# Performance work log

Hardware: AMD Instinct MI355X
Metric: run time of the kernel (lower is better)

The kernel has to match this reference:

```python
import jax, jax.numpy as jnp
import numpy as np

B, Q, S1, S2 = 4, 256, 2048, 2048   # batch, latents, kv lengths
D, H, K, F = 2048, 16, 128, 8192    # embed_dim, heads, key_size, ffn dim
LN_EPS = 1e-5


def _layer_norm(x, scale, offset):
    mu = jnp.mean(x, axis=-1, keepdims=True)
    var = jnp.var(x, axis=-1, keepdims=True)
    return (x - mu) * jax.lax.rsqrt(var + LN_EPS) * scale + offset


def _cross_attention(q_in, kv_in, wq, bq, wk, bk, wv, bv, wo, bo, bias_k, bias_v):
    b, q_len, _ = q_in.shape
    t = kv_in.shape[1]
    qh = (q_in @ wq + bq).reshape(b, q_len, H, K)
    kh = (kv_in @ wk + bk).reshape(b, t, H, K)
    vh = (kv_in @ wv + bv).reshape(b, t, H, K)
    # ESM-style learned bias key/value appended as one extra kv position
    kh = jnp.concatenate([kh, jnp.broadcast_to(bias_k, (b, 1, H, K))], axis=1)
    vh = jnp.concatenate([vh, jnp.broadcast_to(bias_v, (b, 1, H, K))], axis=1)
    scale = jnp.sqrt(jnp.asarray(K, q_in.dtype))
    logits = jnp.einsum('bqhk,bthk->bhqt', qh, kh) / scale  # [B,H,Q,T+1]
    weights = jax.nn.softmax(logits, axis=-1)
    ctx = jnp.einsum('bhqt,bthk->bqhk', weights, vh).reshape(b, q_len, H * K)
    return ctx @ wo + bo


def _forward(x, xf_1, xf_2,
             ln1_scale, ln1_offset, wq1, bq1, wk1, bk1, wv1, bv1, wo1, bo1, bias_k1, bias_v1,
             ln2_scale, ln2_offset, wq2, bq2, wk2, bk2, wv2, bv2, wo2, bo2, bias_k2, bias_v2,
             ln_mlp_scale, ln_mlp_offset, w_fc1, b_fc1, w_fc2, b_fc2):
    res = x
    h = _layer_norm(x, ln1_scale, ln1_offset)
    x = res + _cross_attention(h, xf_1, wq1, bq1, wk1, bk1, wv1, bv1, wo1, bo1, bias_k1, bias_v1)
    res = x
    h = _layer_norm(x, ln2_scale, ln2_offset)
    x = res + _cross_attention(h, xf_2, wq2, bq2, wk2, bk2, wv2, bv2, wo2, bo2, bias_k2, bias_v2)
    h = _layer_norm(x, ln_mlp_scale, ln_mlp_offset)
    h = jax.nn.gelu(h @ w_fc1 + b_fc1, approximate=False) @ w_fc2 + b_fc2
    return x + h


def setup_inputs() -> dict:
    key = jax.random.key(0)
    ks = iter(jax.random.split(key, 64))

    def rn(shape, s=0.02):
        return jax.random.normal(next(ks), shape, jnp.float32) * s

    inp = {
        'x': rn((B, Q, D), 1.0),
        'xf_1': rn((B, S1, D), 1.0),
        'xf_2': rn((B, S2, D), 1.0),
    }
    for i in (1, 2):
        inp[f'ln{i}_scale'] = jnp.ones((D,), jnp.float32)
        inp[f'ln{i}_offset'] = jnp.zeros((D,), jnp.float32)
        inp[f'wq{i}'] = rn((D, H * K))
        inp[f'bq{i}'] = jnp.zeros((H * K,), jnp.float32)
        inp[f'wk{i}'] = rn((D, H * K))
        inp[f'bk{i}'] = jnp.zeros((H * K,), jnp.float32)
        inp[f'wv{i}'] = rn((D, H * K))
        inp[f'bv{i}'] = jnp.zeros((H * K,), jnp.float32)
        inp[f'wo{i}'] = rn((H * K, D))
        inp[f'bo{i}'] = jnp.zeros((D,), jnp.float32)
        inp[f'bias_k{i}'] = rn((1, 1, H, K))
        inp[f'bias_v{i}'] = rn((1, 1, H, K))
    inp['ln_mlp_scale'] = jnp.ones((D,), jnp.float32)
    inp['ln_mlp_offset'] = jnp.zeros((D,), jnp.float32)
    inp['w_fc1'] = rn((D, F))
    inp['b_fc1'] = jnp.zeros((F,), jnp.float32)
    inp['w_fc2'] = rn((F, D))
    inp['b_fc2'] = jnp.zeros((D,), jnp.float32)
    return inp


def reference(x, xf_1, xf_2,
              ln1_scale, ln1_offset, wq1, bq1, wk1, bk1, wv1, bv1, wo1, bo1, bias_k1, bias_v1,
              ln2_scale, ln2_offset, wq2, bq2, wk2, bk2, wv2, bv2, wo2, bo2, bias_k2, bias_v2,
              ln_mlp_scale, ln_mlp_offset, w_fc1, b_fc1, w_fc2, b_fc2):
    return _forward(x, xf_1, xf_2,
                    ln1_scale, ln1_offset, wq1, bq1, wk1, bk1, wv1, bv1, wo1, bo1, bias_k1, bias_v1,
                    ln2_scale, ln2_offset, wq2, bq2, wk2, bk2, wv2, bv2, wo2, bo2, bias_k2, bias_v2,
                    ln_mlp_scale, ln_mlp_offset, w_fc1, b_fc1, w_fc2, b_fc2)
```

## Files before the change

kernel.cpp:

```cpp
#include <hip/hip_runtime.h>

typedef __attribute__((ext_vector_type(8))) short bf16x8;
typedef __attribute__((ext_vector_type(4))) short short4v;
typedef __attribute__((ext_vector_type(4))) float f32x4;

#define D_EMB 2048
#define NQ    256
#define NB    4
#define NS    2048
#define NH    16
#define HK    128
#define FF    8192

__device__ __forceinline__ float b2f(short s) {
  union { unsigned int u; float f; } c;
  c.u = ((unsigned int)(unsigned short)s) << 16;
  return c.f;
}
__device__ __forceinline__ short f2b(float f) {
  union { float f; unsigned int u; } c; c.f = f;
  unsigned int u = c.u;
  u += 0x7FFFu + ((u >> 16) & 1u);
  return (short)(u >> 16);
}
__device__ __forceinline__ void gload_lds16(const short* g, short* l) {
  __builtin_amdgcn_global_load_lds(
      (const __attribute__((address_space(1))) void*)g,
      (__attribute__((address_space(3))) void*)l, 16, 0, 0);
}

__global__ __launch_bounds__(256)
void cvt_kernel(const float* __restrict__ in, short* __restrict__ out, int n8) {
  const int i = (blockIdx.x * 256 + threadIdx.x) * 8;
  if (i >= n8) return;
  f32x4 a = *(const f32x4*)(in + i), b = *(const f32x4*)(in + i + 4);
  bf16x8 t;
#pragma unroll
  for (int j = 0; j < 4; ++j) { t[j] = f2b(a[j]); t[4 + j] = f2b(b[j]); }
  *(bf16x8*)(out + i) = t;
}

__global__ __launch_bounds__(256)
void transpose_kernel(const float* __restrict__ W, short* __restrict__ Wt,
                      int Kd, int N) {
  __shared__ short tile[64][65];
  const int k0 = blockIdx.y * 64, n0 = blockIdx.x * 64;
  const int tid = threadIdx.x;
  const int r = tid >> 2, c4 = (tid & 3) * 16;
#pragma unroll
  for (int i = 0; i < 16; i += 4) {
    f32x4 v = *(const f32x4*)(W + (size_t)(k0 + r) * N + n0 + c4 + i);
#pragma unroll
    for (int j = 0; j < 4; ++j) tile[c4 + i + j][r] = f2b(v[j]);
  }
  __syncthreads();
  bf16x8 o0, o1;
#pragma unroll
  for (int j = 0; j < 8; ++j) { o0[j] = tile[r][c4 + j]; o1[j] = tile[r][c4 + 8 + j]; }
  short* dst = Wt + (size_t)(n0 + r) * Kd + k0 + c4;
  *(bf16x8*)dst = o0;
  *(bf16x8*)(dst + 8) = o1;
}

__global__ __launch_bounds__(256)
void ln_kernel(const float* __restrict__ x, const float* __restrict__ scale,
               const float* __restrict__ offset, short* __restrict__ out) {
  const int row = blockIdx.x, tid = threadIdx.x;
  const float* xr = x + (size_t)row * D_EMB + tid * 8;
  f32x4 v0 = *(const f32x4*)xr;
  f32x4 v1 = *(const f32x4*)(xr + 4);
  float f[8], s = 0.f, sq = 0.f;
#pragma unroll
  for (int i = 0; i < 4; ++i) { f[i] = v0[i]; f[4 + i] = v1[i]; }
#pragma unroll
  for (int i = 0; i < 8; ++i) { s += f[i]; sq += f[i] * f[i]; }
#pragma unroll
  for (int off = 1; off < 64; off <<= 1) {
    s  += __shfl_xor(s, off, 64);
    sq += __shfl_xor(sq, off, 64);
  }
  __shared__ float red[2][4];
  const int w = tid >> 6;
  if ((tid & 63) == 0) { red[0][w] = s; red[1][w] = sq; }
  __syncthreads();
  s  = red[0][0] + red[0][1] + red[0][2] + red[0][3];
  sq = red[1][0] + red[1][1] + red[1][2] + red[1][3];
  const float mu  = s * (1.f / D_EMB);
  const float var = sq * (1.f / D_EMB) - mu * mu;
  const float inv = rsqrtf(var + 1e-5f);
  bf16x8 ov;
#pragma unroll
  for (int i = 0; i < 8; ++i) {
    const int c = tid * 8 + i;
    ov[i] = f2b((f[i] - mu) * inv * scale[c] + offset[c]);
  }
  *(bf16x8*)(out + (size_t)row * D_EMB + tid * 8) = ov;
}

#define FENCE() asm volatile("" ::: "memory")

#define G_STAGE(DB2, DSTOFF, PS0, PS1, KON)                                     \
  gload_lds16((PS0) + (KON), sh + (DB2) * 32768 + (DSTOFF) + tid * 8);          \
  gload_lds16((PS1) + (KON), sh + (DB2) * 32768 + (DSTOFF) + 4096 + tid * 8);

#define PHASE(DB, MG, KH, DSTOFF, PS0, PS1, KON, DOVM)                          \
  {                                                                             \
    const short* _ra = sh + (DB) * 32768 + (KH) * 8192;                         \
    const short* _rb = sh + (DB) * 32768 + 16384 + (KH) * 8192;                 \
    if ((MG) == 0) {                                                            \
      bfrag[0] = *(const bf16x8*)(_rb + boff[0]);                               \
      bfrag[1] = *(const bf16x8*)(_rb + boff[1]);                               \
      bfrag[2] = *(const bf16x8*)(_rb + boff[2]);                               \
      bfrag[3] = *(const bf16x8*)(_rb + boff[3]);                               \
    }                                                                           \
    afrag[0] = *(const bf16x8*)(_ra + aoff[(MG) * 4 + 0]);                      \
    afrag[1] = *(const bf16x8*)(_ra + aoff[(MG) * 4 + 1]);                      \
    afrag[2] = *(const bf16x8*)(_ra + aoff[(MG) * 4 + 2]);                      \
    afrag[3] = *(const bf16x8*)(_ra + aoff[(MG) * 4 + 3]);                      \
    G_STAGE((DB) ^ 1, DSTOFF, PS0, PS1, KON)                                    \
    if (DOVM) asm volatile("s_waitcnt vmcnt(4)" ::: "memory");                  \
    __builtin_amdgcn_s_barrier();                                               \
    FENCE();                                                                    \
    __builtin_amdgcn_s_setprio(1);                                              \
    _Pragma("unroll")                                                           \
    for (int mf = 0; mf < 4; ++mf)                                              \
      _Pragma("unroll")                                                         \
      for (int nf = 0; nf < 4; ++nf)                                            \
        acc[(MG) * 4 + mf][nf] = __builtin_amdgcn_mfma_f32_16x16x32_bf16(       \
            afrag[mf], bfrag[nf], acc[(MG) * 4 + mf][nf], 0, 0, 0);             \
    __builtin_amdgcn_s_setprio(0);                                              \
    __builtin_amdgcn_s_barrier();                                               \
    FENCE();                                                                    \
  }

#define TILE(DB, KON)                                                           \
  PHASE(DB, 0, 0, 0,     pA0, pA1, (KON), 0)                                    \
  PHASE(DB, 1, 0, 16384, pB0, pB1, (KON), 1)                                    \
  PHASE(DB, 0, 1, 8192,  pA0, pA1, (KON) + 32, 0)                               \
  PHASE(DB, 1, 1, 24576, pB0, pB1, (KON) + 32, 1)

template<int EPI, int OUTF, int SPLITK>
__global__ __launch_bounds__(512, 2)
void gemm256_kernel(const short* __restrict__ A, const short* __restrict__ Bt,
                    const float* __restrict__ bias, const float* __restrict__ res,
                    void* __restrict__ Cp, int M, int N, int Kd) {
  __shared__ short sh[65536];
  const int tid = threadIdx.x;
  const int w = tid >> 6, lane = tid & 63;
  const int l15 = lane & 15, quad = lane >> 4;
  const int wm = w >> 2, wn = w & 3;

  const int nTn = N >> 8;
  const int ntiles = (M >> 8) * nTn;
  const int cpx = gridDim.x >> 3;
  const int wid = (blockIdx.x & 7) * cpx + (blockIdx.x >> 3);
  const int tile  = (SPLITK == 1) ? wid : (wid % ntiles);
  const int split = (SPLITK == 1) ? 0   : (wid / ntiles);
  const int Ko = Kd / SPLITK;
  const int ks = split * Ko;
  const int m0 = (tile / nTn) * 256, n0 = (tile % nTn) * 256;

  const int c0 = tid, c1 = 512 + tid;
  const int r0 = ((c0 >> 5) << 3) + (c0 & 7), kb0 = (c0 >> 3) & 3;
  const int r1 = ((c1 >> 5) << 3) + (c1 & 7), kb1 = (c1 >> 3) & 3;
  const short* pA0 = A  + (size_t)(m0 + r0) * Kd + kb0 * 8;
  const short* pA1 = A  + (size_t)(m0 + r1) * Kd + kb1 * 8;
  const short* pB0 = Bt + (size_t)(n0 + r0) * Kd + kb0 * 8;
  const short* pB1 = Bt + (size_t)(n0 + r1) * Kd + kb1 * 8;

  int aoff[8], boff[4];
#pragma unroll
  for (int mf = 0; mf < 8; ++mf) {
    const int r = wm * 128 + mf * 16 + l15;
    aoff[mf] = ((r >> 3) << 8) + (quad << 6) + ((r & 7) << 3);
  }
#pragma unroll
  for (int nf = 0; nf < 4; ++nf) {
    const int r = wn * 64 + nf * 16 + l15;
    boff[nf] = ((r >> 3) << 8) + (quad << 6) + ((r & 7) << 3);
  }

  f32x4 acc[8][4];
#pragma unroll
  for (int mf = 0; mf < 8; ++mf)
#pragma unroll
    for (int nf = 0; nf < 4; ++nf) acc[mf][nf] = (f32x4){0.f, 0.f, 0.f, 0.f};
  bf16x8 afrag[4], bfrag[4];

  const int NT = Ko >> 6;

  G_STAGE(0, 0,     pA0, pA1, ks)
  G_STAGE(0, 16384, pB0, pB1, ks)
  G_STAGE(0, 8192,  pA0, pA1, ks + 32)
  G_STAGE(0, 24576, pB0, pB1, ks + 32)
  asm volatile("s_waitcnt vmcnt(4)" ::: "memory");
  __builtin_amdgcn_s_barrier();
  FENCE();

  for (int kt = 0; kt < NT; kt += 2) {
    const int k1n = ks + (kt + 1) * 64;
    const int k2n = (kt + 2 < NT) ? ks + (kt + 2) * 64 : ks;
    TILE(0, k1n)
    TILE(1, k2n)
  }
  asm volatile("s_waitcnt vmcnt(0) lgkmcnt(0)" ::: "memory");

  if (SPLITK == 1) {
#pragma unroll
    for (int mf = 0; mf < 8; ++mf) {
#pragma unroll
      for (int nf = 0; nf < 4; ++nf) {
        const int gn = n0 + wn * 64 + nf * 16 + l15;
        const float bv = bias[gn];
#pragma unroll
        for (int r = 0; r < 4; ++r) {
          const int gm = m0 + wm * 128 + mf * 16 + quad * 4 + r;
          float v = acc[mf][nf][r] + bv;
          if (EPI == 1) v += res[(size_t)gm * N + gn];
          if (EPI == 2) v = 0.5f * v * (1.f + erff(v * 0.70710678118654752f));
          if (OUTF) ((float*)Cp)[(size_t)gm * N + gn] = v;
          else      ((short*)Cp)[(size_t)gm * N + gn] = f2b(v);
        }
      }
    }
  } else {
    float* po = (float*)Cp + (size_t)split * M * N;
#pragma unroll
    for (int mf = 0; mf < 8; ++mf) {
#pragma unroll
      for (int nf = 0; nf < 4; ++nf) {
        const int gn = n0 + wn * 64 + nf * 16 + l15;
#pragma unroll
        for (int r = 0; r < 4; ++r) {
          const int gm = m0 + wm * 128 + mf * 16 + quad * 4 + r;
          po[(size_t)gm * N + gn] = acc[mf][nf][r];
        }
      }
    }
  }
}

template<int S, int EPI, int OUTF>
__global__ __launch_bounds__(256)
void combine_kernel(const float* __restrict__ po, const float* __restrict__ bias,
                    const float* __restrict__ res, void* __restrict__ out,
                    int M, int N) {
  const size_t i4 = ((size_t)blockIdx.x * 256 + threadIdx.x) * 4;
  if (i4 >= (size_t)M * N) return;
  const int n = (int)(i4 % N);
  f32x4 s = *(const f32x4*)(po + i4);
#pragma unroll
  for (int sp = 1; sp < S; ++sp) {
    const f32x4 p = *(const f32x4*)(po + (size_t)sp * M * N + i4);
#pragma unroll
    for (int j = 0; j < 4; ++j) s[j] += p[j];
  }
  const f32x4 bv = *(const f32x4*)(bias + n);
#pragma unroll
  for (int j = 0; j < 4; ++j) s[j] += bv[j];
  if (EPI == 1) {
    const f32x4 rv = *(const f32x4*)(res + i4);
#pragma unroll
    for (int j = 0; j < 4; ++j) s[j] += rv[j];
  }
  if (EPI == 2) {
#pragma unroll
    for (int j = 0; j < 4; ++j)
      s[j] = 0.5f * s[j] * (1.f + erff(s[j] * 0.70710678118654752f));
  }
  if (OUTF) {
    *(f32x4*)((float*)out + i4) = s;
  } else {
    short4v o;
#pragma unroll
    for (int j = 0; j < 4; ++j) o[j] = f2b(s[j]);
    *(short4v*)((short*)out + i4) = o;
  }
}

__global__ __launch_bounds__(256)
void attn_part_kernel(const short* __restrict__ qh, const short* __restrict__ kh,
                      const short* __restrict__ vh, float* __restrict__ po,
                      float* __restrict__ pml) {
  const int bx = blockIdx.x;
  const int work = (bx & 7) * 128 + (bx >> 3);
  const int bh = work >> 4, sub = work & 15;
  const int qt = sub >> 2, split = sub & 3;
  const int b = bh >> 4, h = bh & 15;
  const int tid = threadIdx.x, w = tid >> 6, lane = tid & 63;
  const int l15 = lane & 15, quad = lane >> 4;
  const int q0 = qt * 64 + w * 16;

  __shared__ short ldsK[32 * 128];
  __shared__ short ldsV[128 * 32];
  __shared__ short ldsP[4 * 16 * 32];

  const float sc = 0.08838834764831845f;

  bf16x8 aq[4];
  {
    const short* qrow = qh + ((size_t)(b * 256 + q0 + l15)) * D_EMB + h * 128;
#pragma unroll
    for (int s = 0; s < 4; ++s)
      aq[s] = *(const bf16x8*)(qrow + s * 32 + quad * 8);
  }

  f32x4 o[8];
  float m_run[4], l_run[4];
#pragma unroll
  for (int dt = 0; dt < 8; ++dt) o[dt] = (f32x4){0.f, 0.f, 0.f, 0.f};
#pragma unroll
  for (int r = 0; r < 4; ++r) { m_run[r] = -INFINITY; l_run[r] = 0.f; }

  const int srow = tid >> 4;
  const int j = tid & 15;
  const int ksw = (j ^ (srow & 7)) * 8;
  const int t_beg = split * 512;

  for (int t0 = t_beg; t0 < t_beg + 512; t0 += 32) {
    __syncthreads();
    const size_t kb0 = ((size_t)(b * NS + t0 + srow)) * D_EMB + h * 128;
    const size_t kb1 = kb0 + (size_t)16 * D_EMB;
    gload_lds16(kh + kb0 + ksw, ldsK + tid * 8);
    gload_lds16(kh + kb1 + ksw, ldsK + 2048 + tid * 8);
    {
      bf16x8 v0 = *(const bf16x8*)(vh + kb0 + j * 8);
      bf16x8 v1 = *(const bf16x8*)(vh + kb1 + j * 8);
#pragma unroll
      for (int i = 0; i < 8; ++i) {
        const int d = j * 8 + i;
        const int swz = ((d >> 3) & 3) << 4;
        char* base = (char*)ldsV + (d << 6);
        *(short*)(base + ((srow << 1) ^ swz))        = v0[i];
        *(short*)(base + (((srow + 16) << 1) ^ swz)) = v1[i];
      }
    }
    __syncthreads();

    f32x4 s0 = (f32x4){0.f, 0.f, 0.f, 0.f}, s1 = (f32x4){0.f, 0.f, 0.f, 0.f};
    const int kswr = (l15 & 7) << 4;
#pragma unroll
    for (int s = 0; s < 4; ++s) {
      const int cb = s * 64 + quad * 16;
      bf16x8 k0f = *(bf16x8*)((char*)ldsK + (l15 << 8)        + (cb ^ kswr));
      bf16x8 k1f = *(bf16x8*)((char*)ldsK + ((16 + l15) << 8) + (cb ^ kswr));
      s0 = __builtin_amdgcn_mfma_f32_16x16x32_bf16(aq[s], k0f, s0, 0, 0, 0);
      s1 = __builtin_amdgcn_mfma_f32_16x16x32_bf16(aq[s], k1f, s1, 0, 0, 0);
    }

    float alpha_r[4];
#pragma unroll
    for (int r = 0; r < 4; ++r) {
      const float v0 = s0[r] * sc, v1 = s1[r] * sc;
      float mx = fmaxf(v0, v1);
#pragma unroll
      for (int off = 1; off < 16; off <<= 1) mx = fmaxf(mx, __shfl_xor(mx, off, 16));
      const float m_new = fmaxf(m_run[r], mx);
      const float p0 = expf(v0 - m_new), p1 = expf(v1 - m_new);
      float rs = p0 + p1;
#pragma unroll
      for (int off = 1; off < 16; off <<= 1) rs += __shfl_xor(rs, off, 16);
      alpha_r[r] = expf(m_run[r] - m_new);
      l_run[r] = l_run[r] * alpha_r[r] + rs;
      m_run[r] = m_new;
      const int prow = quad * 4 + r;
      const int psw = ((prow >> 1) & 3) << 4;
      char* pb = (char*)ldsP + w * 1024 + (prow << 6);
      *(short*)(pb + ((l15 << 1) ^ psw))        = f2b(p0);
      *(short*)(pb + (((16 + l15) << 1) ^ psw)) = f2b(p1);
    }
#pragma unroll
    for (int dt = 0; dt < 8; ++dt)
#pragma unroll
      for (int r = 0; r < 4; ++r) o[dt][r] *= alpha_r[r];

    bf16x8 pf = *(bf16x8*)((char*)ldsP + w * 1024 + (l15 << 6) +
                           ((quad << 4) ^ (((l15 >> 1) & 3) << 4)));
#pragma unroll
    for (int dt = 0; dt < 8; ++dt) {
      const int drow = dt * 16 + l15;
      bf16x8 vf = *(bf16x8*)((char*)ldsV + (drow << 6) +
                             ((quad << 4) ^ (((drow >> 3) & 3) << 4)));
      o[dt] = __builtin_amdgcn_mfma_f32_16x16x32_bf16(pf, vf, o[dt], 0, 0, 0);
    }
  }

  const int orow_base = (bh * 4 + qt) * 64 + w * 16;
#pragma unroll
  for (int dt = 0; dt < 8; ++dt)
#pragma unroll
    for (int r = 0; r < 4; ++r) {
      const size_t orow = (size_t)(orow_base + quad * 4 + r);
      po[(orow * 4 + split) * 128 + dt * 16 + l15] = o[dt][r];
    }
  if (l15 == 0) {
#pragma unroll
    for (int r = 0; r < 4; ++r) {
      const size_t orow = (size_t)(orow_base + quad * 4 + r);
      pml[(orow * 4 + split) * 2]     = m_run[r];
      pml[(orow * 4 + split) * 2 + 1] = l_run[r];
    }
  }
}

__global__ __launch_bounds__(256)
void attn_combine_kernel(const short* __restrict__ qh, const float* __restrict__ bias_k,
                         const float* __restrict__ bias_v, const float* __restrict__ po,
                         const float* __restrict__ pml, short* __restrict__ ctx) {
  const int tid = threadIdx.x, w = tid >> 6, lane = tid & 63;
  const int task = blockIdx.x * 4 + w;
  const int bh = task >> 8, qr = task & 255;
  const int b = bh >> 4, h = bh & 15;
  const int d0 = lane * 2;
  const float sc = 0.08838834764831845f;

  const short* qrow = qh + ((size_t)(b * 256 + qr)) * D_EMB + h * 128 + d0;
  const unsigned int qv = *(const unsigned int*)qrow;
  const float q0 = b2f((short)(qv & 0xffffu));
  const float q1 = b2f((short)(qv >> 16));
  const float2 bk = *(const float2*)(bias_k + h * 128 + d0);
  float le = q0 * bk.x + q1 * bk.y;
#pragma unroll
  for (int off = 1; off < 64; off <<= 1) le += __shfl_xor(le, off, 64);
  le *= sc;

  const float* pm = pml + (size_t)task * 8;
  float m[4], l[4];
#pragma unroll
  for (int s = 0; s < 4; ++s) { m[s] = pm[s * 2]; l[s] = pm[s * 2 + 1]; }
  float mt = le;
#pragma unroll
  for (int s = 0; s < 4; ++s) mt = fmaxf(mt, m[s]);

  const float pe = expf(le - mt);
  const float2 bv = *(const float2*)(bias_v + h * 128 + d0);
  float acc0 = pe * bv.x, acc1 = pe * bv.y;
  float lt = pe;
#pragma unroll
  for (int s = 0; s < 4; ++s) {
    const float es = expf(m[s] - mt);
    lt += l[s] * es;
    const float2 op = *(const float2*)(po + ((size_t)task * 4 + s) * 128 + d0);
    acc0 += es * op.x;
    acc1 += es * op.y;
  }
  const float inv = 1.f / lt;
  const unsigned int pack =
      ((unsigned int)(unsigned short)f2b(acc1 * inv) << 16) |
      (unsigned short)f2b(acc0 * inv);
  *(unsigned int*)(ctx + ((size_t)(b * 256 + qr)) * D_EMB + h * 128 + d0) = pack;
}

extern "C" void kernel_launch(void* const* d_in, const int* in_sizes, int n_in,
                              void* d_out, int out_size, void* d_ws, size_t ws_size,
                              hipStream_t stream) {
  const float* x   = (const float*)d_in[0];
  const float* xf1 = (const float*)d_in[1];
  const float* xf2 = (const float*)d_in[2];
  const float* L1[12]; const float* L2[12];
  for (int j = 0; j < 12; ++j) { L1[j] = (const float*)d_in[3 + j]; L2[j] = (const float*)d_in[15 + j]; }
  const float* ln_mlp_s = (const float*)d_in[27];
  const float* ln_mlp_o = (const float*)d_in[28];
  const float* w_fc1    = (const float*)d_in[29];
  const float* b_fc1    = (const float*)d_in[30];
  const float* w_fc2    = (const float*)d_in[31];
  const float* b_fc2    = (const float*)d_in[32];
  float* out = (float*)d_out;

  const size_t SZ_XQ  = (size_t)NB * NQ * D_EMB;
  const size_t SZ_KV  = (size_t)NB * NS * D_EMB;

  float* x1   = (float*)d_ws;
  float* x2   = x1 + SZ_XQ;
  short* h_ln = (short*)(x2 + SZ_XQ);
  short* qh   = h_ln + SZ_XQ;
  short* ctxb = qh + SZ_XQ;
  short* kh   = ctxb + SZ_XQ;
  short* vh   = kh + SZ_KV;
  short* xfb  = vh + SZ_KV;
  short* Wt   = xfb + SZ_KV;
  short* fc1b = kh;
  float* po   = (float*)Wt;
  float* pml  = (float*)h_ln;
  float* pk1  = (float*)kh;
  float* pk2  = (float*)vh;

  const dim3 blk(256);
  const dim3 blk5(512);
  const dim3 g_kv256((NB * NS / 256) * (D_EMB / 256));
  const dim3 g_sk(256);
  const dim3 g_skf1(256);
  const dim3 g_cb2(2048);
  const dim3 g_cb8(8192);
  const dim3 g_tw(D_EMB / 64, D_EMB / 64);
  const dim3 g_tf1(FF / 64, D_EMB / 64);
  const dim3 g_tf2(D_EMB / 64, FF / 64);
  const int  g_cvt = (int)(SZ_KV / 8 / 256);

  cvt_kernel<<<g_cvt, blk, 0, stream>>>(xf1, xfb, (int)SZ_KV);
  ln_kernel<<<NB * NQ, blk, 0, stream>>>(x, L1[0], L1[1], h_ln);
  transpose_kernel<<<g_tw, blk, 0, stream>>>(L1[2], Wt, D_EMB, D_EMB);
  gemm256_kernel<0,0,8><<<g_sk, blk5, 0, stream>>>(h_ln, Wt, nullptr, nullptr, pk1, NB * NQ, D_EMB, D_EMB);
  combine_kernel<8,0,0><<<g_cb2, blk, 0, stream>>>(pk1, L1[3], nullptr, qh, NB * NQ, D_EMB);
  transpose_kernel<<<g_tw, blk, 0, stream>>>(L1[4], Wt, D_EMB, D_EMB);
  gemm256_kernel<0,0,1><<<g_kv256, blk5, 0, stream>>>(xfb, Wt, L1[5], nullptr, kh, NB * NS, D_EMB, D_EMB);
  transpose_kernel<<<g_tw, blk, 0, stream>>>(L1[6], Wt, D_EMB, D_EMB);
  gemm256_kernel<0,0,1><<<g_kv256, blk5, 0, stream>>>(xfb, Wt, L1[7], nullptr, vh, NB * NS, D_EMB, D_EMB);
  attn_part_kernel<<<1024, blk, 0, stream>>>(qh, kh, vh, po, pml);
  attn_combine_kernel<<<4096, blk, 0, stream>>>(qh, L1[10], L1[11], po, pml, ctxb);
  transpose_kernel<<<g_tw, blk, 0, stream>>>(L1[8], Wt, D_EMB, D_EMB);
  gemm256_kernel<0,0,8><<<g_sk, blk5, 0, stream>>>(ctxb, Wt, nullptr, nullptr, pk1, NB * NQ, D_EMB, D_EMB);
  combine_kernel<8,1,1><<<g_cb2, blk, 0, stream>>>(pk1, L1[9], x, x1, NB * NQ, D_EMB);

  cvt_kernel<<<g_cvt, blk, 0, stream>>>(xf2, xfb, (int)SZ_KV);
  ln_kernel<<<NB * NQ, blk, 0, stream>>>(x1, L2[0], L2[1], h_ln);
  transpose_kernel<<<g_tw, blk, 0, stream>>>(L2[2], Wt, D_EMB, D_EMB);
  gemm256_kernel<0,0,8><<<g_sk, blk5, 0, stream>>>(h_ln, Wt, nullptr, nullptr, pk1, NB * NQ, D_EMB, D_EMB);
  combine_kernel<8,0,0><<<g_cb2, blk, 0, stream>>>(pk1, L2[3], nullptr, qh, NB * NQ, D_EMB);
  transpose_kernel<<<g_tw, blk, 0, stream>>>(L2[4], Wt, D_EMB, D_EMB);
  gemm256_kernel<0,0,1><<<g_kv256, blk5, 0, stream>>>(xfb, Wt, L2[5], nullptr, kh, NB * NS, D_EMB, D_EMB);
  transpose_kernel<<<g_tw, blk, 0, stream>>>(L2[6], Wt, D_EMB, D_EMB);
  gemm256_kernel<0,0,1><<<g_kv256, blk5, 0, stream>>>(xfb, Wt, L2[7], nullptr, vh, NB * NS, D_EMB, D_EMB);
  attn_part_kernel<<<1024, blk, 0, stream>>>(qh, kh, vh, po, pml);
  attn_combine_kernel<<<4096, blk, 0, stream>>>(qh, L2[10], L2[11], po, pml, ctxb);
  transpose_kernel<<<g_tw, blk, 0, stream>>>(L2[8], Wt, D_EMB, D_EMB);
  gemm256_kernel<0,0,8><<<g_sk, blk5, 0, stream>>>(ctxb, Wt, nullptr, nullptr, pk1, NB * NQ, D_EMB, D_EMB);
  combine_kernel<8,1,1><<<g_cb2, blk, 0, stream>>>(pk1, L2[9], x1, x2, NB * NQ, D_EMB);

  ln_kernel<<<NB * NQ, blk, 0, stream>>>(x2, ln_mlp_s, ln_mlp_o, h_ln);
  transpose_kernel<<<g_tf1, blk, 0, stream>>>(w_fc1, Wt, D_EMB, FF);
  gemm256_kernel<0,0,2><<<g_skf1, blk5, 0, stream>>>(h_ln, Wt, nullptr, nullptr, pk2, NB * NQ, FF, D_EMB);
  combine_kernel<2,2,0><<<g_cb8, blk, 0, stream>>>(pk2, b_fc1, nullptr, fc1b, NB * NQ, FF);
  transpose_kernel<<<g_tf2, blk, 0, stream>>>(w_fc2, Wt, FF, D_EMB);
  gemm256_kernel<0,0,8><<<g_sk, blk5, 0, stream>>>(fc1b, Wt, nullptr, nullptr, pk2, NB * NQ, D_EMB, FF);
  combine_kernel<8,1,1><<<g_cb2, blk, 0, stream>>>(pk2, b_fc2, x2, out, NB * NQ, D_EMB);
}
```

Measured before the change: 1.173 ms.

## Write V transposed from GEMM epilogue and streamline attention softmax rescaling

The V projection GEMM gains a transposed epilogue that stages its tile through LDS and writes V as [b, h*d, t]. The attention kernel can then copy V tiles straight into LDS with async loads instead of scattering shorts one at a time. The attention loop also skips rescaling the running max unless a score exceeds it by a threshold. The row sum is now accumulated with an MFMA against a ones vector rather than through shuffle reductions. The aim is to cut the cost of the V shuffle and of the per-tile softmax bookkeeping, in exchange for a more complex GEMM epilogue and a less strict max update that relies on headroom for the exponentials.

```diff
diff --git a/kernel.cpp b/kernel.cpp
--- a/kernel.cpp
+++ b/kernel.cpp
@@ -139,7 +139,7 @@
   PHASE(DB, 0, 1, 8192,  pA0, pA1, (KON) + 32, 0)                               \
   PHASE(DB, 1, 1, 24576, pB0, pB1, (KON) + 32, 1)
 
-template<int EPI, int OUTF, int SPLITK>
+template<int EPI, int OUTF, int SPLITK, int TRANSP>
 __global__ __launch_bounds__(512, 2)
 void gemm256_kernel(const short* __restrict__ A, const short* __restrict__ Bt,
                     const float* __restrict__ bias, const float* __restrict__ res,
@@ -205,7 +205,35 @@
   }
   asm volatile("s_waitcnt vmcnt(0) lgkmcnt(0)" ::: "memory");
 
-  if (SPLITK == 1) {
+  if (TRANSP) {
+    FENCE();
+    const int bb = m0 >> 11;
+    const int t0t = m0 & 2047;
+#pragma unroll
+    for (int mf = 0; mf < 8; ++mf) {
+      const int m_dw = wm * 64 + mf * 8 + quad * 2;
+#pragma unroll
+      for (int nf = 0; nf < 4; ++nf) {
+        const int n_loc = wn * 64 + nf * 16 + l15;
+        const float bv = bias[n0 + n_loc];
+        short4v pk;
+#pragma unroll
+        for (int r = 0; r < 4; ++r) pk[r] = f2b(acc[mf][nf][r] + bv);
+        const int m_sw = m_dw ^ ((n_loc & 3) << 2);
+        *(short4v*)(sh + n_loc * 256 + (m_sw << 1)) = pk;
+      }
+    }
+    __syncthreads();
+#pragma unroll
+    for (int it = 0; it < 16; ++it) {
+      const int n_r = (tid >> 5) + it * 16;
+      const int m_blk = tid & 31;
+      const int m_sw = (m_blk << 2) ^ ((n_r & 3) << 2);
+      const bf16x8 v = *(const bf16x8*)(sh + n_r * 256 + (m_sw << 1));
+      short* dst = (short*)Cp + ((size_t)(bb * 2048) + n0 + n_r) * 2048 + t0t + m_blk * 8;
+      *(bf16x8*)dst = v;
+    }
+  } else if (SPLITK == 1) {
 #pragma unroll
     for (int mf = 0; mf < 8; ++mf) {
 #pragma unroll
@@ -280,7 +308,7 @@
 
 __global__ __launch_bounds__(256)
 void attn_part_kernel(const short* __restrict__ qh, const short* __restrict__ kh,
-                      const short* __restrict__ vh, float* __restrict__ po,
+                      const short* __restrict__ vt, float* __restrict__ po,
                       float* __restrict__ pml) {
   const int bx = blockIdx.x;
   const int work = (bx & 7) * 128 + (bx >> 3);
@@ -296,6 +324,7 @@
   __shared__ short ldsP[4 * 16 * 32];
 
   const float sc = 0.08838834764831845f;
+  const float THR = 8.f;
 
   bf16x8 aq[4];
   {
@@ -304,17 +333,24 @@
     for (int s = 0; s < 4; ++s)
       aq[s] = *(const bf16x8*)(qrow + s * 32 + quad * 8);
   }
+  bf16x8 ones;
+#pragma unroll
+  for (int i = 0; i < 8; ++i) ones[i] = (short)0x3F80;
 
   f32x4 o[8];
-  float m_run[4], l_run[4];
+  f32x4 o_sum = (f32x4){0.f, 0.f, 0.f, 0.f};
+  float m_run[4];
 #pragma unroll
   for (int dt = 0; dt < 8; ++dt) o[dt] = (f32x4){0.f, 0.f, 0.f, 0.f};
 #pragma unroll
-  for (int r = 0; r < 4; ++r) { m_run[r] = -INFINITY; l_run[r] = 0.f; }
+  for (int r = 0; r < 4; ++r) m_run[r] = -INFINITY;
 
   const int srow = tid >> 4;
-  const int j = tid & 15;
-  const int ksw = (j ^ (srow & 7)) * 8;
+  const int ksw = ((tid & 15) ^ (srow & 7)) * 8;
+  const short* vt_base = vt + ((size_t)(b * 2048 + h * 128)) * 2048;
+  const short* pv0 = vt_base + (size_t)(tid >> 2) * 2048 + (tid & 3) * 8;
+  const short* pv1 = pv0 + (size_t)64 * 2048;
+
   const int t_beg = split * 512;
 
   for (int t0 = t_beg; t0 < t_beg + 512; t0 += 32) {
@@ -323,18 +359,8 @@
     const size_t kb1 = kb0 + (size_t)16 * D_EMB;
     gload_lds16(kh + kb0 + ksw, ldsK + tid * 8);
     gload_lds16(kh + kb1 + ksw, ldsK + 2048 + tid * 8);
-    {
-      bf16x8 v0 = *(const bf16x8*)(vh + kb0 + j * 8);
-      bf16x8 v1 = *(const bf16x8*)(vh + kb1 + j * 8);
-#pragma unroll
-      for (int i = 0; i < 8; ++i) {
-        const int d = j * 8 + i;
-        const int swz = ((d >> 3) & 3) << 4;
-        char* base = (char*)ldsV + (d << 6);
-        *(short*)(base + ((srow << 1) ^ swz))        = v0[i];
-        *(short*)(base + (((srow + 16) << 1) ^ swz)) = v1[i];
-      }
-    }
+    gload_lds16(pv0 + t0, ldsV + tid * 8);
+    gload_lds16(pv1 + t0, ldsV + 2048 + tid * 8);
     __syncthreads();
 
     f32x4 s0 = (f32x4){0.f, 0.f, 0.f, 0.f}, s1 = (f32x4){0.f, 0.f, 0.f, 0.f};
@@ -348,39 +374,47 @@
       s1 = __builtin_amdgcn_mfma_f32_16x16x32_bf16(aq[s], k1f, s1, 0, 0, 0);
     }
 
-    float alpha_r[4];
+    int okl = 1;
 #pragma unroll
     for (int r = 0; r < 4; ++r) {
-      const float v0 = s0[r] * sc, v1 = s1[r] * sc;
-      float mx = fmaxf(v0, v1);
-#pragma unroll
-      for (int off = 1; off < 16; off <<= 1) mx = fmaxf(mx, __shfl_xor(mx, off, 16));
-      const float m_new = fmaxf(m_run[r], mx);
-      const float p0 = expf(v0 - m_new), p1 = expf(v1 - m_new);
-      float rs = p0 + p1;
-#pragma unroll
-      for (int off = 1; off < 16; off <<= 1) rs += __shfl_xor(rs, off, 16);
-      alpha_r[r] = expf(m_run[r] - m_new);
-      l_run[r] = l_run[r] * alpha_r[r] + rs;
-      m_run[r] = m_new;
+      s0[r] *= sc; s1[r] *= sc;
+      okl &= (s0[r] <= m_run[r] + THR) & (s1[r] <= m_run[r] + THR);
+    }
+    if (!__all(okl)) {
+      float alpha_r[4];
+#pragma unroll
+      for (int r = 0; r < 4; ++r) {
+        float mx = fmaxf(s0[r], s1[r]);
+#pragma unroll
+        for (int off = 1; off < 16; off <<= 1) mx = fmaxf(mx, __shfl_xor(mx, off, 16));
+        const float m_new = fmaxf(m_run[r], mx);
+        alpha_r[r] = expf(m_run[r] - m_new);
+        m_run[r] = m_new;
+      }
+#pragma unroll
+      for (int dt = 0; dt < 8; ++dt)
+#pragma unroll
+        for (int r = 0; r < 4; ++r) o[dt][r] *= alpha_r[r];
+#pragma unroll
+      for (int r = 0; r < 4; ++r) o_sum[r] *= alpha_r[r];
+    }
+#pragma unroll
+    for (int r = 0; r < 4; ++r) {
+      const float p0 = expf(s0[r] - m_run[r]);
+      const float p1 = expf(s1[r] - m_run[r]);
       const int prow = quad * 4 + r;
       const int psw = ((prow >> 1) & 3) << 4;
       char* pb = (char*)ldsP + w * 1024 + (prow << 6);
       *(short*)(pb + ((l15 << 1) ^ psw))        = f2b(p0);
       *(short*)(pb + (((16 + l15) << 1) ^ psw)) = f2b(p1);
     }
-#pragma unroll
-    for (int dt = 0; dt < 8; ++dt)
-#pragma unroll
-      for (int r = 0; r < 4; ++r) o[dt][r] *= alpha_r[r];
 
     bf16x8 pf = *(bf16x8*)((char*)ldsP + w * 1024 + (l15 << 6) +
                            ((quad << 4) ^ (((l15 >> 1) & 3) << 4)));
+    o_sum = __builtin_amdgcn_mfma_f32_16x16x32_bf16(pf, ones, o_sum, 0, 0, 0);
 #pragma unroll
     for (int dt = 0; dt < 8; ++dt) {
-      const int drow = dt * 16 + l15;
-      bf16x8 vf = *(bf16x8*)((char*)ldsV + (drow << 6) +
-                             ((quad << 4) ^ (((drow >> 3) & 3) << 4)));
+      bf16x8 vf = *(const bf16x8*)(ldsV + (dt * 16 + l15) * 32 + quad * 8);
       o[dt] = __builtin_amdgcn_mfma_f32_16x16x32_bf16(pf, vf, o[dt], 0, 0, 0);
     }
   }
@@ -398,7 +432,7 @@
     for (int r = 0; r < 4; ++r) {
       const size_t orow = (size_t)(orow_base + quad * 4 + r);
       pml[(orow * 4 + split) * 2]     = m_run[r];
-      pml[(orow * 4 + split) * 2 + 1] = l_run[r];
+      pml[(orow * 4 + split) * 2 + 1] = o_sum[r];
     }
   }
 }
@@ -489,7 +523,6 @@
   const dim3 blk5(512);
   const dim3 g_kv256((NB * NS / 256) * (D_EMB / 256));
   const dim3 g_sk(256);
-  const dim3 g_skf1(256);
   const dim3 g_cb2(2048);
   const dim3 g_cb8(8192);
   const dim3 g_tw(D_EMB / 64, D_EMB / 64);
@@ -500,38 +533,38 @@
   cvt_kernel<<<g_cvt, blk, 0, stream>>>(xf1, xfb, (int)SZ_KV);
   ln_kernel<<<NB * NQ, blk, 0, stream>>>(x, L1[0], L1[1], h_ln);
   transpose_kernel<<<g_tw, blk, 0, stream>>>(L1[2], Wt, D_EMB, D_EMB);
-  gemm256_kernel<0,0,8><<<g_sk, blk5, 0, stream>>>(h_ln, Wt, nullptr, nullptr, pk1, NB * NQ, D_EMB, D_EMB);
+  gemm256_kernel<0,0,8,0><<<g_sk, blk5, 0, stream>>>(h_ln, Wt, nullptr, nullptr, pk1, NB * NQ, D_EMB, D_EMB);
   combine_kernel<8,0,0><<<g_cb2, blk, 0, stream>>>(pk1, L1[3], nullptr, qh, NB * NQ, D_EMB);
   transpose_kernel<<<g_tw, blk, 0, stream>>>(L1[4], Wt, D_EMB, D_EMB);
-  gemm256_kernel<0,0,1><<<g_kv256, blk5, 0, stream>>>(xfb, Wt, L1[5], nullptr, kh, NB * NS, D_EMB, D_EMB);
+  gemm256_kernel<0,0,1,0><<<g_kv256, blk5, 0, stream>>>(xfb, Wt, L1[5], nullptr, kh, NB * NS, D_EMB, D_EMB);
   transpose_kernel<<<g_tw, blk, 0, stream>>>(L1[6], Wt, D_EMB, D_EMB);
-  gemm256_kernel<0,0,1><<<g_kv256, blk5, 0, stream>>>(xfb, Wt, L1[7], nullptr, vh, NB * NS, D_EMB, D_EMB);
+  gemm256_kernel<0,0,1,1><<<g_kv256, blk5, 0, stream>>>(xfb, Wt, L1[7], nullptr, vh, NB * NS, D_EMB, D_EMB);
   attn_part_kernel<<<1024, blk, 0, stream>>>(qh, kh, vh, po, pml);
   attn_combine_kernel<<<4096, blk, 0, stream>>>(qh, L1[10], L1[11], po, pml, ctxb);
   transpose_kernel<<<g_tw, blk, 0, stream>>>(L1[8], Wt, D_EMB, D_EMB);
-  gemm256_kernel<0,0,8><<<g_sk, blk5, 0, stream>>>(ctxb, Wt, nullptr, nullptr, pk1, NB * NQ, D_EMB, D_EMB);
+  gemm256_kernel<0,0,8,0><<<g_sk, blk5, 0, stream>>>(ctxb, Wt, nullptr, nullptr, pk1, NB * NQ, D_EMB, D_EMB);
   combine_kernel<8,1,1><<<g_cb2, blk, 0, stream>>>(pk1, L1[9], x, x1, NB * NQ, D_EMB);
 
   cvt_kernel<<<g_cvt, blk, 0, stream>>>(xf2, xfb, (int)SZ_KV);
   ln_kernel<<<NB * NQ, blk, 0, stream>>>(x1, L2[0], L2[1], h_ln);
   transpose_kernel<<<g_tw, blk, 0, stream>>>(L2[2], Wt, D_EMB, D_EMB);
-  gemm256_kernel<0,0,8><<<g_sk, blk5, 0, stream>>>(h_ln, Wt, nullptr, nullptr, pk1, NB * NQ, D_EMB, D_EMB);
+  gemm256_kernel<0,0,8,0><<<g_sk, blk5, 0, stream>>>(h_ln, Wt, nullptr, nullptr, pk1, NB * NQ, D_EMB, D_EMB);
   combine_kernel<8,0,0><<<g_cb2, blk, 0, stream>>>(pk1, L2[3], nullptr, qh, NB * NQ, D_EMB);
   transpose_kernel<<<g_tw, blk, 0, stream>>>(L2[4], Wt, D_EMB, D_EMB);
-  gemm256_kernel<0,0,1><<<g_kv256, blk5, 0, stream>>>(xfb, Wt, L2[5], nullptr, kh, NB * NS, D_EMB, D_EMB);
+  gemm256_kernel<0,0,1,0><<<g_kv256, blk5, 0, stream>>>(xfb, Wt, L2[5], nullptr, kh, NB * NS, D_EMB, D_EMB);
   transpose_kernel<<<g_tw, blk, 0, stream>>>(L2[6], Wt, D_EMB, D_EMB);
-  gemm256_kernel<0,0,1><<<g_kv256, blk5, 0, stream>>>(xfb, Wt, L2[7], nullptr, vh, NB * NS, D_EMB, D_EMB);
+  gemm256_kernel<0,0,1,1><<<g_kv256, blk5, 0, stream>>>(xfb, Wt, L2[7], nullptr, vh, NB * NS, D_EMB, D_EMB);
   attn_part_kernel<<<1024, blk, 0, stream>>>(qh, kh, vh, po, pml);
   attn_combine_kernel<<<4096, blk, 0, stream>>>(qh, L2[10], L2[11], po, pml, ctxb);
   transpose_kernel<<<g_tw, blk, 0, stream>>>(L2[8], Wt, D_EMB, D_EMB);
-  gemm256_kernel<0,0,8><<<g_sk, blk5, 0, stream>>>(ctxb, Wt, nullptr, nullptr, pk1, NB * NQ, D_EMB, D_EMB);
+  gemm256_kernel<0,0,8,0><<<g_sk, blk5, 0, stream>>>(ctxb, Wt, nullptr, nullptr, pk1, NB * NQ, D_EMB, D_EMB);
   combine_kernel<8,1,1><<<g_cb2, blk, 0, stream>>>(pk1, L2[9], x1, x2, NB * NQ, D_EMB);
 
   ln_kernel<<<NB * NQ, blk, 0, stream>>>(x2, ln_mlp_s, ln_mlp_o, h_ln);
   transpose_kernel<<<g_tf1, blk, 0, stream>>>(w_fc1, Wt, D_EMB, FF);
-  gemm256_kernel<0,0,2><<<g_skf1, blk5, 0, stream>>>(h_ln, Wt, nullptr, nullptr, pk2, NB * NQ, FF, D_EMB);
+  gemm256_kernel<0,0,2,0><<<g_sk, blk5, 0, stream>>>(h_ln, Wt, nullptr, nullptr, pk2, NB * NQ, FF, D_EMB);
   combine_kernel<2,2,0><<<g_cb8, blk, 0, stream>>>(pk2, b_fc1, nullptr, fc1b, NB * NQ, FF);
   transpose_kernel<<<g_tf2, blk, 0, stream>>>(w_fc2, Wt, FF, D_EMB);
-  gemm256_kernel<0,0,8><<<g_sk, blk5, 0, stream>>>(fc1b, Wt, nullptr, nullptr, pk2, NB * NQ, D_EMB, FF);
+  gemm256_kernel<0,0,8,0><<<g_sk, blk5, 0, stream>>>(fc1b, Wt, nullptr, nullptr, pk2, NB * NQ, D_EMB, FF);
   combine_kernel<8,1,1><<<g_cb2, blk, 0, stream>>>(pk2, b_fc2, x2, out, NB * NQ, D_EMB);
 }
```

New measurement: 1.112 ms. 1.05x faster.
